# Kernel optimization log

Hardware: AMD Instinct MI355X
Metric: run time of the kernel (lower is better)

Reference implementation:

```python
import jax, jax.numpy as jnp
import numpy as np
import math

NEG_INF = -1000000000.0
D_EMBED = 1024
D_K = 1024
N_HEADS = 16
D_H = D_EMBED // N_HEADS


def setup_inputs() -> dict:
    key = jax.random.key(0)
    ks = jax.random.split(key, 12)
    B, S = 2, 2048
    s = 0.02
    return {
        "embed": jax.random.normal(ks[0], (B, S, D_EMBED), dtype=jnp.float32),
        "key": jax.random.normal(ks[1], (B, S, D_K), dtype=jnp.float32),
        "attn_mask": jax.random.randint(ks[2], (B, S, S), 0, 2, dtype=jnp.int32),
        "Wq": jax.random.normal(ks[3], (D_EMBED, D_EMBED), dtype=jnp.float32) * s,
        "bq": jnp.zeros((D_EMBED,), dtype=jnp.float32),
        "Wk": jax.random.normal(ks[4], (D_EMBED, D_K), dtype=jnp.float32) * s,
        "bk": jnp.zeros((D_EMBED,), dtype=jnp.float32),
        "Wv": jax.random.normal(ks[5], (D_EMBED, D_K), dtype=jnp.float32) * s,
        "bv": jnp.zeros((D_EMBED,), dtype=jnp.float32),
        "Wo": jax.random.normal(ks[6], (D_EMBED, D_EMBED), dtype=jnp.float32) * s,
        "bo": jnp.zeros((D_EMBED,), dtype=jnp.float32),
    }


def _alibi_bias(seq_len: int, n_heads: int) -> jnp.ndarray:
    # symmetric |i-j| distances, slopes 2^-(8k/H) for k=1..H
    r = jnp.arange(seq_len)
    pos = jnp.abs(r[None, :] - r[:, None]).astype(jnp.float32)  # [S, S]
    step = 8.0 / n_heads
    ms = 2.0 ** (-jnp.arange(step, 8.0 + step, step, dtype=jnp.float32))  # [H]
    return ms[:, None, None] * pos[None, :, :]  # [H, S, S]


def reference(embed, key, attn_mask, Wq, bq, Wk, bk, Wv, bv, Wo, bo):
    B, Sq, _ = embed.shape
    Sk = key.shape[1]
    Q = embed @ Wq.T + bq          # [B, Sq, D]
    K = key @ Wk.T + bk            # [B, Sk, D]
    V = key @ Wv.T + bv            # [B, Sk, D]
    Qh = Q.reshape(B, Sq, N_HEADS, D_H).transpose(0, 2, 1, 3)  # [B, H, Sq, d_h]
    Kh = K.reshape(B, Sk, N_HEADS, D_H).transpose(0, 2, 1, 3)
    Vh = V.reshape(B, Sk, N_HEADS, D_H).transpose(0, 2, 1, 3)
    attn = jnp.einsum("bhqd,bhkd->bhqk", Qh, Kh)
    # ALiBi bias subtracted BEFORE scaling (as in source)
    attn = attn - _alibi_bias(Sq, N_HEADS)[None]
    attn = attn * (1.0 / math.sqrt(D_EMBED))  # note: scale uses d_embed, not d_h
    attn = jnp.where(attn_mask[:, None, :, :] == 0, NEG_INF, attn)
    attn = jax.nn.softmax(attn, axis=-1)
    out = jnp.einsum("bhqk,bhkd->bhqd", attn, Vh)
    out = out.transpose(0, 2, 1, 3).reshape(B, Sq, D_EMBED)
    return out @ Wo.T + bo
```

## Files before the change

### kernel.cpp

```cpp
#include <hip/hip_runtime.h>


typedef _Float16 f16;
typedef __attribute__((ext_vector_type(8))) _Float16 f16x8;
typedef __attribute__((ext_vector_type(4))) _Float16 f16x4;
typedef __attribute__((ext_vector_type(4))) float f32x4;
typedef unsigned long long u64;
typedef unsigned int u32;

#define MFMA16 __builtin_amdgcn_mfma_f32_16x16x32_f16

__global__ __launch_bounds__(256) void k_convert(
    const float* __restrict__ embed, const float* __restrict__ key,
    const float* __restrict__ wq, const float* __restrict__ wk,
    const float* __restrict__ wv, const float* __restrict__ wo,
    f16* __restrict__ xe, f16* __restrict__ xk,
    f16* __restrict__ wqh, f16* __restrict__ wkh,
    f16* __restrict__ wvh, f16* __restrict__ woh)
{
    long g = (long)blockIdx.x * 256 + threadIdx.x;
    const float* src; f16* dst; long off;
    if (g < 524288)       { src = embed; dst = xe; off = g; }
    else if (g < 1048576) { src = key;   dst = xk; off = g - 524288; }
    else {
        long t = g - 1048576; int wi = (int)(t >> 17); off = t & 131071;
        if (wi == 0)      { src = wq; dst = wqh; }
        else if (wi == 1) { src = wk; dst = wkh; }
        else if (wi == 2) { src = wv; dst = wvh; }
        else              { src = wo; dst = woh; }
    }
    const float4* s4 = (const float4*)src;
    float4 a = s4[off * 2], b = s4[off * 2 + 1];
    f16x8 o;
    o[0]=(f16)a.x; o[1]=(f16)a.y; o[2]=(f16)a.z; o[3]=(f16)a.w;
    o[4]=(f16)b.x; o[5]=(f16)b.y; o[6]=(f16)b.z; o[7]=(f16)b.w;
    *(f16x8*)(dst + off * 8) = o;
}

__global__ __launch_bounds__(256) void k_packmask(
    const int* __restrict__ mask, u64* __restrict__ bits)
{
    int gw = (blockIdx.x * 256 + threadIdx.x) >> 6;
    int lane = threadIdx.x & 63;
    const int* row = mask + (long)gw * 2048;
    u64* out = bits + (long)gw * 32;
    #pragma unroll 4
    for (int c = 0; c < 32; ++c) {
        int v = row[c * 64 + lane];
        u64 b = __ballot(v != 0);
        if (lane == 0) out[c] = b;
    }
}

__global__ __launch_bounds__(256) void k_qkv(
    const f16* __restrict__ xe, const f16* __restrict__ xk,
    const f16* __restrict__ wqh, const f16* __restrict__ wkh, const f16* __restrict__ wvh,
    const float* __restrict__ bq, const float* __restrict__ bk, const float* __restrict__ bv,
    f16* __restrict__ Qh, f16* __restrict__ Kh, f16* __restrict__ Vt)
{
    int bid = blockIdx.x;
    int which = bid >> 8;
    int rr_ = bid & 255;
    int tm = rr_ >> 3, tn = rr_ & 7;
    const f16* X = (which == 0) ? xe : xk;
    const f16* W = (which == 0) ? wqh : (which == 1) ? wkh : wvh;
    const float* bias = (which == 0) ? bq : (which == 1) ? bk : bv;

    __shared__ f16 smem[128 * 136];
    f16* la = smem;
    f16* lb = smem + 128 * 64;

    int tid = threadIdx.x;
    int lane = tid & 63, wid = tid >> 6;
    int wr = wid >> 1, wc = wid & 1;
    int lm = lane & 15, qd = lane >> 4;

    f32x4 acc[4][4];
    #pragma unroll
    for (int i = 0; i < 4; i++)
        #pragma unroll
        for (int j = 0; j < 4; j++) acc[i][j] = (f32x4)0.0f;

    int m0 = tm * 128, n0 = tn * 128;

    for (int kt = 0; kt < 16; ++kt) {
        int k0 = kt * 64;
        __syncthreads();
        #pragma unroll
        for (int t = 0; t < 4; ++t) {
            int cid = tid + t * 256;
            int row = cid >> 3;
            int cg = cid & 7;
            int sw = cg ^ (row & 7);
            *(f16x8*)&la[row * 64 + sw * 8] =
                *(const f16x8*)&X[(long)(m0 + row) * 1024 + k0 + cg * 8];
            *(f16x8*)&lb[row * 64 + sw * 8] =
                *(const f16x8*)&W[(long)(n0 + row) * 1024 + k0 + cg * 8];
        }
        __syncthreads();
        #pragma unroll
        for (int ks = 0; ks < 2; ++ks) {
            f16x8 af[4], bfr[4];
            #pragma unroll
            for (int i = 0; i < 4; i++) {
                int m = 64 * wr + 16 * i + lm;
                int g = (ks * 4 + qd) ^ (m & 7);
                af[i] = *(const f16x8*)&la[m * 64 + g * 8];
                int n = 64 * wc + 16 * i + lm;
                int g2 = (ks * 4 + qd) ^ (n & 7);
                bfr[i] = *(const f16x8*)&lb[n * 64 + g2 * 8];
            }
            #pragma unroll
            for (int i = 0; i < 4; i++)
                #pragma unroll
                for (int j = 0; j < 4; j++)
                    acc[i][j] = MFMA16(af[i], bfr[j], acc[i][j], 0, 0, 0);
        }
    }

    if (which == 2) {
        #pragma unroll
        for (int j = 0; j < 4; j++) {
            int n = n0 + 64 * wc + 16 * j + lm;
            float bb = bias[n];
            int h = n >> 6, d = n & 63;
            #pragma unroll
            for (int i = 0; i < 4; i++) {
                int mbase = m0 + 64 * wr + 16 * i + 4 * qd;
                f16x4 pk;
                #pragma unroll
                for (int r = 0; r < 4; ++r) pk[r] = (f16)(acc[i][j][r] + bb);
                int b = mbase >> 11, s = mbase & 2047;
                *(f16x4*)&Vt[(((long)(b * 16 + h)) * 64 + d) * 2048 + s] = pk;
            }
        }
    } else {
        f16* dst = (which == 0) ? Qh : Kh;
        __syncthreads();
        #pragma unroll
        for (int j = 0; j < 4; j++) {
            int col = 64 * wc + 16 * j + lm;
            float bb = bias[n0 + col];
            #pragma unroll
            for (int i = 0; i < 4; i++) {
                int row = 64 * wr + 16 * i + 4 * qd;
                #pragma unroll
                for (int r = 0; r < 4; ++r)
                    smem[(row + r) * 136 + col] = (f16)(acc[i][j][r] + bb);
            }
        }
        __syncthreads();
        #pragma unroll
        for (int t = 0; t < 8; ++t) {
            int ci = tid + t * 256;
            int row = ci >> 4, cg = ci & 15;
            f16x8 v = *(const f16x8*)&smem[row * 136 + cg * 8];
            int m = m0 + row;
            int b = m >> 11, s = m & 2047;
            int h = (n0 >> 6) + (cg >> 3);
            int d0 = (cg & 7) * 8;
            *(f16x8*)&dst[(((long)(b * 16 + h)) * 2048 + s) * 64 + d0] = v;
        }
    }
}

__global__ __launch_bounds__(256, 2) void k_attn(
    const f16* __restrict__ Qh, const f16* __restrict__ Kh, const f16* __restrict__ Vt,
    const u64* __restrict__ mbits, f16* __restrict__ O)
{
    int bid = blockIdx.x;
    int qt = bid & 15;
    int h = (bid >> 4) & 15;
    int b = bid >> 8;
    int q0 = qt * 128;

    const f16* Qg = Qh + ((long)(b * 16 + h)) * 2048 * 64;
    const f16* Kg = Kh + ((long)(b * 16 + h)) * 2048 * 64;
    const f16* Vg = Vt + ((long)(b * 16 + h)) * 64 * 2048;
    const u64* Mg = mbits + ((long)(b * 2048 + q0)) * 32;

    __shared__ f16 ks[128 * 64];
    __shared__ f16 vs[64 * 128];
    __shared__ f16 ps[4][32 * 128];

    int tid = threadIdx.x, lane = tid & 63, wid = tid >> 6;
    int lm = lane & 15, qd = lane >> 4;

    f16x8 aq[2][2];
    #pragma unroll
    for (int ksi = 0; ksi < 2; ++ksi)
        #pragma unroll
        for (int i = 0; i < 2; ++i)
            aq[ksi][i] = *(const f16x8*)&Qg[(long)(q0 + 32 * wid + 16 * i + lm) * 64
                                            + ksi * 32 + qd * 8];

    f32x4 oacc[2][4], lacc[2];
    #pragma unroll
    for (int i = 0; i < 2; i++) {
        lacc[i] = (f32x4)0.0f;
        #pragma unroll
        for (int c = 0; c < 4; c++) oacc[i][c] = (f32x4)0.0f;
    }
    f16x8 vone;
    #pragma unroll
    for (int j = 0; j < 8; j++) vone[j] = (f16)1.0f;

    const float c1 = 0.0450842252f;
    float c2 = __builtin_amdgcn_exp2f(-0.5f * (float)(h + 1)) * c1;
    const float c3 = 5.7707801634f;

    for (int kt = 0; kt < 16; ++kt) {
        int k0 = kt * 128;
        __syncthreads();
        #pragma unroll
        for (int t = 0; t < 4; ++t) {
            int cid = tid + t * 256;
            int row = cid >> 3, cg = cid & 7;
            int sw = cg ^ (row & 7);
            *(f16x8*)&ks[row * 64 + sw * 8] =
                *(const f16x8*)&Kg[(long)(k0 + row) * 64 + cg * 8];
            int vrow = cid >> 4, vg = cid & 15;
            int vsw = vg ^ (vrow & 7);
            *(f16x8*)&vs[vrow * 128 + vsw * 8] =
                *(const f16x8*)&Vg[(long)vrow * 2048 + k0 + vg * 8];
        }
        __syncthreads();

        u64 mw0[2][4], mw1[2][4];
        #pragma unroll
        for (int i = 0; i < 2; i++)
            #pragma unroll
            for (int r = 0; r < 4; r++) {
                const u64* mp = Mg + (long)(32 * wid + 16 * i + 4 * qd + r) * 32 + kt * 2;
                mw0[i][r] = mp[0];
                mw1[i][r] = mp[1];
            }

        f32x4 sacc[2][8];
        #pragma unroll
        for (int i = 0; i < 2; i++)
            #pragma unroll
            for (int c = 0; c < 8; c++) sacc[i][c] = (f32x4)0.0f;
        #pragma unroll
        for (int ksi = 0; ksi < 2; ++ksi) {
            #pragma unroll
            for (int c = 0; c < 8; c++) {
                int n = 16 * c + lm;
                int g = (ksi * 4 + qd) ^ (n & 7);
                f16x8 bk_ = *(const f16x8*)&ks[n * 64 + g * 8];
                sacc[0][c] = MFMA16(aq[ksi][0], bk_, sacc[0][c], 0, 0, 0);
                sacc[1][c] = MFMA16(aq[ksi][1], bk_, sacc[1][c], 0, 0, 0);
            }
        }

        #pragma unroll
        for (int i = 0; i < 2; i++) {
            #pragma unroll
            for (int r = 0; r < 4; r++) {
                int lr = 32 * wid + 16 * i + 4 * qd + r;
                u32 sh[4];
                sh[0] = ((u32)mw0[i][r]) >> lm;
                sh[1] = ((u32)(mw0[i][r] >> 32)) >> lm;
                sh[2] = ((u32)mw1[i][r]) >> lm;
                sh[3] = ((u32)(mw1[i][r] >> 32)) >> lm;
                float dfb = (float)((q0 + lr) - k0 - lm);
                int pr = 16 * i + 4 * qd + r;
                #pragma unroll
                for (int c = 0; c < 8; c++) {
                    float t = fmaf(sacc[i][c][r], c1, -c3);
                    float u = fmaf(fabsf(dfb - 16.0f * c), -c2, t);
                    u32 keep = (sh[c >> 1] >> ((c & 1) * 16)) & 1u;
                    float p = __builtin_amdgcn_exp2f(keep ? u : -1e30f);
                    int g = ((2 * c + (lm >> 3)) ^ (pr & 7));
                    ps[wid][pr * 128 + g * 8 + (lm & 7)] = (f16)p;
                }
            }
        }

        #pragma unroll
        for (int k4 = 0; k4 < 4; ++k4) {
            f16x8 pa[2];
            #pragma unroll
            for (int i = 0; i < 2; i++) {
                int m = 16 * i + lm;
                int g = (k4 * 4 + qd) ^ (m & 7);
                pa[i] = *(const f16x8*)&ps[wid][m * 128 + g * 8];
            }
            #pragma unroll
            for (int c = 0; c < 4; c++) {
                int d = 16 * c + lm;
                int g = (k4 * 4 + qd) ^ (d & 7);
                f16x8 vb = *(const f16x8*)&vs[d * 128 + g * 8];
                oacc[0][c] = MFMA16(pa[0], vb, oacc[0][c], 0, 0, 0);
                oacc[1][c] = MFMA16(pa[1], vb, oacc[1][c], 0, 0, 0);
            }
            lacc[0] = MFMA16(pa[0], vone, lacc[0], 0, 0, 0);
            lacc[1] = MFMA16(pa[1], vone, lacc[1], 0, 0, 0);
        }
    }

    #pragma unroll
    for (int i = 0; i < 2; i++) {
        #pragma unroll
        for (int r = 0; r < 4; r++) {
            int lr = 32 * wid + 16 * i + 4 * qd + r;
            float linv = 1.0f / fmaxf(lacc[i][r], 1e-30f);
            long rowbase = ((long)(b * 2048 + q0 + lr)) * 1024 + h * 64;
            #pragma unroll
            for (int c = 0; c < 4; c++) {
                int d = 16 * c + lm;
                O[rowbase + d] = (f16)(oacc[i][c][r] * linv);
            }
        }
    }
}

__global__ __launch_bounds__(256) void k_proj(
    const f16* __restrict__ Oh, const f16* __restrict__ woh,
    const float* __restrict__ bo, float* __restrict__ out)
{
    int bid = blockIdx.x;
    int tm = bid >> 3, tn = bid & 7;

    __shared__ f16 la[128 * 64];
    __shared__ f16 lb[128 * 64];

    int tid = threadIdx.x;
    int lane = tid & 63, wid = tid >> 6;
    int wr = wid >> 1, wc = wid & 1;
    int lm = lane & 15, qd = lane >> 4;

    f32x4 acc[4][4];
    #pragma unroll
    for (int i = 0; i < 4; i++)
        #pragma unroll
        for (int j = 0; j < 4; j++) acc[i][j] = (f32x4)0.0f;

    int m0 = tm * 128, n0 = tn * 128;

    for (int kt = 0; kt < 16; ++kt) {
        int k0 = kt * 64;
        __syncthreads();
        #pragma unroll
        for (int t = 0; t < 4; ++t) {
            int cid = tid + t * 256;
            int row = cid >> 3;
            int cg = cid & 7;
            int sw = cg ^ (row & 7);
            *(f16x8*)&la[row * 64 + sw * 8] =
                *(const f16x8*)&Oh[(long)(m0 + row) * 1024 + k0 + cg * 8];
            *(f16x8*)&lb[row * 64 + sw * 8] =
                *(const f16x8*)&woh[(long)(n0 + row) * 1024 + k0 + cg * 8];
        }
        __syncthreads();
        #pragma unroll
        for (int ks = 0; ks < 2; ++ks) {
            f16x8 af[4], bfr[4];
            #pragma unroll
            for (int i = 0; i < 4; i++) {
                int m = 64 * wr + 16 * i + lm;
                int g = (ks * 4 + qd) ^ (m & 7);
                af[i] = *(const f16x8*)&la[m * 64 + g * 8];
                int n = 64 * wc + 16 * i + lm;
                int g2 = (ks * 4 + qd) ^ (n & 7);
                bfr[i] = *(const f16x8*)&lb[n * 64 + g2 * 8];
            }
            #pragma unroll
            for (int i = 0; i < 4; i++)
                #pragma unroll
                for (int j = 0; j < 4; j++)
                    acc[i][j] = MFMA16(af[i], bfr[j], acc[i][j], 0, 0, 0);
        }
    }

    #pragma unroll
    for (int j = 0; j < 4; j++) {
        int n = n0 + 64 * wc + 16 * j + lm;
        float bb = bo[n];
        #pragma unroll
        for (int i = 0; i < 4; i++) {
            int mbase = m0 + 64 * wr + 16 * i + 4 * qd;
            #pragma unroll
            for (int r = 0; r < 4; ++r)
                out[(long)(mbase + r) * 1024 + n] = acc[i][j][r] + bb;
        }
    }
}

extern "C" void kernel_launch(void* const* d_in, const int* in_sizes, int n_in,
                              void* d_out, int out_size, void* d_ws, size_t ws_size,
                              hipStream_t stream)
{
    const float* embed = (const float*)d_in[0];
    const float* key   = (const float*)d_in[1];
    const int*   mask  = (const int*)d_in[2];
    const float* Wq = (const float*)d_in[3];
    const float* bq = (const float*)d_in[4];
    const float* Wk = (const float*)d_in[5];
    const float* bk = (const float*)d_in[6];
    const float* Wv = (const float*)d_in[7];
    const float* bv = (const float*)d_in[8];
    const float* Wo = (const float*)d_in[9];
    const float* bo = (const float*)d_in[10];

    char* ws = (char*)d_ws;
    f16* xe  = (f16*)(ws + 0);
    f16* xk  = (f16*)(ws + 8388608);
    f16* wqh = (f16*)(ws + 16777216);
    f16* wkh = (f16*)(ws + 18874368);
    f16* wvh = (f16*)(ws + 20971520);
    f16* woh = (f16*)(ws + 23068672);
    f16* Qh  = (f16*)(ws + 25165824);
    f16* Kh  = (f16*)(ws + 33554432);
    f16* Vt  = (f16*)(ws + 41943040);
    f16* Oh  = (f16*)(ws + 50331648);
    u64* mb  = (u64*)(ws + 58720256);
    float* out = (float*)d_out;

    k_convert<<<6144, 256, 0, stream>>>(embed, key, Wq, Wk, Wv, Wo,
                                        xe, xk, wqh, wkh, wvh, woh);
    k_packmask<<<1024, 256, 0, stream>>>(mask, mb);
    k_qkv<<<768, 256, 0, stream>>>(xe, xk, wqh, wkh, wvh, bq, bk, bv, Qh, Kh, Vt);
    k_attn<<<512, 256, 0, stream>>>(Qh, Kh, Vt, mb, Oh);
    k_proj<<<256, 256, 0, stream>>>(Oh, woh, bo, out);
}
```

Before: 316.8 us.

## Use 8 waves of 16 query rows per attention block with transposed score tiles

The attention kernel moves from 256 threads (4 waves × 32 query rows) to 512 threads (8 waves × 16 query rows). This halves per-wave accumulator registers and raises the number of resident waves for latency hiding. The score MFMA now takes K as the A operand, so each lane holds one query row and four consecutive keys. That lets each lane read its own row's mask words, extract a 4-bit nibble per tile, and write P to shared memory as packed f16x4. The trade-off is that each wave reuses the shared K/V tiles over fewer query rows, roughly doubling LDS read traffic per flop.

```diff
diff --git a/kernel.cpp b/kernel.cpp
--- a/kernel.cpp
+++ b/kernel.cpp
@@ -164,7 +164,7 @@
     }
 }
 
-__global__ __launch_bounds__(256, 2) void k_attn(
+__global__ __launch_bounds__(512, 4) void k_attn(
     const f16* __restrict__ Qh, const f16* __restrict__ Kh, const f16* __restrict__ Vt,
     const u64* __restrict__ mbits, f16* __restrict__ O)
 {
@@ -177,44 +177,40 @@
     const f16* Qg = Qh + ((long)(b * 16 + h)) * 2048 * 64;
     const f16* Kg = Kh + ((long)(b * 16 + h)) * 2048 * 64;
     const f16* Vg = Vt + ((long)(b * 16 + h)) * 64 * 2048;
-    const u64* Mg = mbits + ((long)(b * 2048 + q0)) * 32;
 
     __shared__ f16 ks[128 * 64];
     __shared__ f16 vs[64 * 128];
-    __shared__ f16 ps[4][32 * 128];
+    __shared__ f16 ps[8][16 * 128];
 
     int tid = threadIdx.x, lane = tid & 63, wid = tid >> 6;
     int lm = lane & 15, qd = lane >> 4;
 
-    f16x8 aq[2][2];
+    int qrow = q0 + 16 * wid + lm;
+    const u64* Mrow = mbits + ((long)(b * 2048) + qrow) * 32;
+
+    f16x8 aq[2];
     #pragma unroll
     for (int ksi = 0; ksi < 2; ++ksi)
-        #pragma unroll
-        for (int i = 0; i < 2; ++i)
-            aq[ksi][i] = *(const f16x8*)&Qg[(long)(q0 + 32 * wid + 16 * i + lm) * 64
-                                            + ksi * 32 + qd * 8];
-
-    f32x4 oacc[2][4], lacc[2];
-    #pragma unroll
-    for (int i = 0; i < 2; i++) {
-        lacc[i] = (f32x4)0.0f;
-        #pragma unroll
-        for (int c = 0; c < 4; c++) oacc[i][c] = (f32x4)0.0f;
-    }
+        aq[ksi] = *(const f16x8*)&Qg[(long)qrow * 64 + ksi * 32 + qd * 8];
+
+    f32x4 oacc[4], lacc;
+    #pragma unroll
+    for (int c = 0; c < 4; c++) oacc[c] = (f32x4)0.0f;
+    lacc = (f32x4)0.0f;
     f16x8 vone;
     #pragma unroll
     for (int j = 0; j < 8; j++) vone[j] = (f16)1.0f;
 
     const float c1 = 0.0450842252f;
-    float c2 = __builtin_amdgcn_exp2f(-0.5f * (float)(h + 1)) * c1;
+    float negc2 = -__builtin_amdgcn_exp2f(-0.5f * (float)(h + 1)) * c1;
     const float c3 = 5.7707801634f;
 
     for (int kt = 0; kt < 16; ++kt) {
         int k0 = kt * 128;
         __syncthreads();
         #pragma unroll
-        for (int t = 0; t < 4; ++t) {
-            int cid = tid + t * 256;
+        for (int t = 0; t < 2; ++t) {
+            int cid = tid + t * 512;
             int row = cid >> 3, cg = cid & 7;
             int sw = cg ^ (row & 7);
             *(f16x8*)&ks[row * 64 + sw * 8] =
@@ -226,92 +222,66 @@
         }
         __syncthreads();
 
-        u64 mw0[2][4], mw1[2][4];
-        #pragma unroll
-        for (int i = 0; i < 2; i++)
-            #pragma unroll
-            for (int r = 0; r < 4; r++) {
-                const u64* mp = Mg + (long)(32 * wid + 16 * i + 4 * qd + r) * 32 + kt * 2;
-                mw0[i][r] = mp[0];
-                mw1[i][r] = mp[1];
-            }
-
-        f32x4 sacc[2][8];
-        #pragma unroll
-        for (int i = 0; i < 2; i++)
-            #pragma unroll
-            for (int c = 0; c < 8; c++) sacc[i][c] = (f32x4)0.0f;
+        u64 w0 = Mrow[kt * 2], w1 = Mrow[kt * 2 + 1];
+
+        f32x4 sacc[8];
+        #pragma unroll
+        for (int c = 0; c < 8; c++) sacc[c] = (f32x4)0.0f;
         #pragma unroll
         for (int ksi = 0; ksi < 2; ++ksi) {
             #pragma unroll
             for (int c = 0; c < 8; c++) {
-                int n = 16 * c + lm;
-                int g = (ksi * 4 + qd) ^ (n & 7);
-                f16x8 bk_ = *(const f16x8*)&ks[n * 64 + g * 8];
-                sacc[0][c] = MFMA16(aq[ksi][0], bk_, sacc[0][c], 0, 0, 0);
-                sacc[1][c] = MFMA16(aq[ksi][1], bk_, sacc[1][c], 0, 0, 0);
-            }
-        }
-
-        #pragma unroll
-        for (int i = 0; i < 2; i++) {
-            #pragma unroll
-            for (int r = 0; r < 4; r++) {
-                int lr = 32 * wid + 16 * i + 4 * qd + r;
-                u32 sh[4];
-                sh[0] = ((u32)mw0[i][r]) >> lm;
-                sh[1] = ((u32)(mw0[i][r] >> 32)) >> lm;
-                sh[2] = ((u32)mw1[i][r]) >> lm;
-                sh[3] = ((u32)(mw1[i][r] >> 32)) >> lm;
-                float dfb = (float)((q0 + lr) - k0 - lm);
-                int pr = 16 * i + 4 * qd + r;
-                #pragma unroll
-                for (int c = 0; c < 8; c++) {
-                    float t = fmaf(sacc[i][c][r], c1, -c3);
-                    float u = fmaf(fabsf(dfb - 16.0f * c), -c2, t);
-                    u32 keep = (sh[c >> 1] >> ((c & 1) * 16)) & 1u;
-                    float p = __builtin_amdgcn_exp2f(keep ? u : -1e30f);
-                    int g = ((2 * c + (lm >> 3)) ^ (pr & 7));
-                    ps[wid][pr * 128 + g * 8 + (lm & 7)] = (f16)p;
-                }
-            }
+                int kr = 16 * c + lm;
+                int g = (ksi * 4 + qd) ^ (kr & 7);
+                f16x8 ak = *(const f16x8*)&ks[kr * 64 + g * 8];
+                sacc[c] = MFMA16(ak, aq[ksi], sacc[c], 0, 0, 0);
+            }
+        }
+
+        float qmkb = (float)(qrow - k0 - 4 * qd);
+        int shb = 4 * qd;
+        #pragma unroll
+        for (int c = 0; c < 8; c++) {
+            u32 nib = (u32)(((c < 4) ? w0 : w1) >> (16 * (c & 3) + shb)) & 15u;
+            float qmkc = qmkb - 16.0f * (float)c;
+            float p[4];
+            #pragma unroll
+            for (int r = 0; r < 4; ++r) {
+                float t2 = fmaf(sacc[c][r], c1, -c3);
+                float dd = qmkc - (float)r;
+                float u = fmaf(fabsf(dd), negc2, t2);
+                u = ((nib >> r) & 1u) ? u : -1e30f;
+                p[r] = __builtin_amdgcn_exp2f(u);
+            }
+            f16x4 pk;
+            #pragma unroll
+            for (int r = 0; r < 4; ++r) pk[r] = (f16)p[r];
+            int g8 = (2 * c + (qd >> 1)) ^ (lm & 7);
+            *(f16x4*)&ps[wid][lm * 128 + g8 * 8 + (qd & 1) * 4] = pk;
         }
 
         #pragma unroll
         for (int k4 = 0; k4 < 4; ++k4) {
-            f16x8 pa[2];
-            #pragma unroll
-            for (int i = 0; i < 2; i++) {
-                int m = 16 * i + lm;
-                int g = (k4 * 4 + qd) ^ (m & 7);
-                pa[i] = *(const f16x8*)&ps[wid][m * 128 + g * 8];
-            }
-            #pragma unroll
-            for (int c = 0; c < 4; c++) {
-                int d = 16 * c + lm;
+            int gp = (k4 * 4 + qd) ^ (lm & 7);
+            f16x8 pa = *(const f16x8*)&ps[wid][lm * 128 + gp * 8];
+            #pragma unroll
+            for (int cc = 0; cc < 4; ++cc) {
+                int d = 16 * cc + lm;
                 int g = (k4 * 4 + qd) ^ (d & 7);
                 f16x8 vb = *(const f16x8*)&vs[d * 128 + g * 8];
-                oacc[0][c] = MFMA16(pa[0], vb, oacc[0][c], 0, 0, 0);
-                oacc[1][c] = MFMA16(pa[1], vb, oacc[1][c], 0, 0, 0);
-            }
-            lacc[0] = MFMA16(pa[0], vone, lacc[0], 0, 0, 0);
-            lacc[1] = MFMA16(pa[1], vone, lacc[1], 0, 0, 0);
-        }
-    }
-
-    #pragma unroll
-    for (int i = 0; i < 2; i++) {
-        #pragma unroll
-        for (int r = 0; r < 4; r++) {
-            int lr = 32 * wid + 16 * i + 4 * qd + r;
-            float linv = 1.0f / fmaxf(lacc[i][r], 1e-30f);
-            long rowbase = ((long)(b * 2048 + q0 + lr)) * 1024 + h * 64;
-            #pragma unroll
-            for (int c = 0; c < 4; c++) {
-                int d = 16 * c + lm;
-                O[rowbase + d] = (f16)(oacc[i][c][r] * linv);
-            }
-        }
+                oacc[cc] = MFMA16(pa, vb, oacc[cc], 0, 0, 0);
+            }
+            lacc = MFMA16(pa, vone, lacc, 0, 0, 0);
+        }
+    }
+
+    #pragma unroll
+    for (int r = 0; r < 4; ++r) {
+        float linv = 1.0f / fmaxf(lacc[r], 1e-30f);
+        long rowbase = ((long)(b * 2048 + q0 + 16 * wid + 4 * qd + r)) * 1024 + h * 64;
+        #pragma unroll
+        for (int cc = 0; cc < 4; ++cc)
+            O[rowbase + 16 * cc + lm] = (f16)(oacc[cc][r] * linv);
     }
 }
 
@@ -421,6 +391,6 @@
                                         xe, xk, wqh, wkh, wvh, woh);
     k_packmask<<<1024, 256, 0, stream>>>(mask, mb);
     k_qkv<<<768, 256, 0, stream>>>(xe, xk, wqh, wkh, wvh, bq, bk, bv, Qh, Kh, Vt);
-    k_attn<<<512, 256, 0, stream>>>(Qh, Kh, Vt, mb, Oh);
+    k_attn<<<512, 512, 0, stream>>>(Qh, Kh, Vt, mb, Oh);
     k_proj<<<256, 256, 0, stream>>>(Oh, woh, bo, out);
 }
```

New measurement: 275.5 us. -13.0%, faster.
